# Performance work log

Measured on AMD Instinct MI355X. Metric: run time of the kernel, lower is better.

Reference implementation:

```python
import jax, jax.numpy as jnp
import numpy as np

B, S, D, H = 2, 2048, 1024, 16
HD = D // H  # head_dim = 64


def setup_inputs() -> dict:
    key = jax.random.key(0)
    ks = jax.random.split(key, 12)
    xav = (2.0 / (D + D)) ** 0.5  # xavier_normal std for square Linear
    q = jax.random.normal(ks[0], (B, S, D), jnp.float32)
    k = jax.random.normal(ks[1], (B, S, D), jnp.float32)
    v = jax.random.normal(ks[2], (B, S, D), jnp.float32)
    Wq = jax.random.normal(ks[3], (D, D), jnp.float32) * xav
    Wk = jax.random.normal(ks[4], (D, D), jnp.float32) * xav
    Wv = jax.random.normal(ks[5], (D, D), jnp.float32) * xav
    bq = jnp.zeros((D,), jnp.float32)
    bk = jnp.zeros((D,), jnp.float32)
    bv = jnp.zeros((D,), jnp.float32)
    # valid-prefix padding masks (True = valid token); key 0 always valid so
    # no causal softmax row is fully masked (avoids NaN, matches real usage).
    klen = jax.random.randint(ks[6], (B,), S // 2, S + 1)
    qlen = jax.random.randint(ks[7], (B,), S // 2, S + 1)
    pos = jnp.arange(S)
    key_padding_mask = pos[None, :] < klen[:, None]
    query_padding_mask = pos[None, :] < qlen[:, None]
    return {
        "q": q, "k": k, "v": v,
        "Wq": Wq, "bq": bq, "Wk": Wk, "bk": bk, "Wv": Wv, "bv": bv,
        "key_padding_mask": key_padding_mask,
        "query_padding_mask": query_padding_mask,
    }


def _proj_split(x, W, b, n_heads):
    # Linear (y = x W^T + b) then split heads: [B,S,D] -> [B,H,S,hd]
    bsz, sq, dm = x.shape
    hd = dm // n_heads
    y = x @ W.T + b
    return y.reshape(bsz, sq, n_heads, hd).transpose(0, 2, 1, 3)


def reference(q, k, v, Wq, bq, Wk, bk, Wv, bv, key_padding_mask, query_padding_mask):
    bsz, sq, dm = q.shape
    sk = k.shape[1]
    Q = _proj_split(q, Wq, bq, H)  # [B,H,Sq,hd]
    K = _proj_split(k, Wk, bk, H)  # [B,H,Sk,hd]
    V = _proj_split(v, Wv, bv, H)  # [B,H,Sk,hd]
    scale = 1.0 / jnp.sqrt(jnp.asarray(Q.shape[-1], Q.dtype))
    scores = jnp.einsum('bhqd,bhkd->bhqk', Q, K) * scale  # [B,H,Sq,Sk]
    # key padding: -inf where key invalid
    scores = jnp.where(key_padding_mask[:, None, None, :], scores, -jnp.inf)
    # causal: -inf strictly above the diagonal
    causal_ok = jnp.tril(jnp.ones((sq, sk), bool))
    scores = jnp.where(causal_ok[None, None, :, :], scores, -jnp.inf)
    attn = jax.nn.softmax(scores, axis=-1)
    # q_mask: zero out rows for padded queries (post-softmax, as in source)
    attn = jnp.where(query_padding_mask[:, None, :, None], attn, 0.0)
    # dropout p=0.0 -> identity
    out = jnp.einsum('bhqk,bhkd->bhqd', attn, V)
    out = out.transpose(0, 2, 1, 3).reshape(bsz, sq, dm)
    return out + q
```

## Files before the change

### kernel.cpp

```cpp
#include <hip/hip_runtime.h>
#include <stdint.h>

#define BATCH 2
#define SEQ 2048
#define DMODEL 1024
#define NHEAD 16
#define HDIM 64
#define CVT_BLOCKS 15360

typedef __attribute__((ext_vector_type(8))) short bf16x8;
typedef __attribute__((ext_vector_type(4))) float f32x4;

__device__ __forceinline__ unsigned short f2bf(float f) {
  unsigned int u = __float_as_uint(f);
  u += 0x7fffu + ((u >> 16) & 1u);
  return (unsigned short)(u >> 16);
}
__device__ __forceinline__ unsigned int pk2bf(float a, float b) {
  return __builtin_amdgcn_perm(__float_as_uint(b) + 0x8000u,
                               __float_as_uint(a) + 0x8000u, 0x07060302u);
}
__device__ __forceinline__ void async_copy16(const void* g, void* l) {
  __builtin_amdgcn_global_load_lds(
      (const __attribute__((address_space(1))) void*)g,
      (__attribute__((address_space(3))) void*)l, 16, 0, 0);
}

__global__ __launch_bounds__(256) void cvt_all(
    const float* __restrict__ q, const float* __restrict__ k,
    const float* __restrict__ v, const float* __restrict__ Wq,
    const float* __restrict__ Wk, const float* __restrict__ Wv,
    unsigned short* __restrict__ dst,
    const unsigned char* __restrict__ kp, const unsigned char* __restrict__ qp,
    int* __restrict__ lens) {
  if (blockIdx.x == CVT_BLOCKS) {
    const int t = threadIdx.x, wave = t >> 6, lane = t & 63;
    const unsigned char* base = (wave < 2) ? kp : qp;
    const int b = wave & 1;
    const bool bytefmt = (base[1] != 0);
    int cnt = 0;
    if (bytefmt) {
      const uint4* p = (const uint4*)(base + (size_t)b * SEQ);
#pragma unroll
      for (int g = 0; g < 2; g++) {
        const uint4 x = p[g * 64 + lane];
        const unsigned int w[4] = {x.x, x.y, x.z, x.w};
#pragma unroll
        for (int i = 0; i < 4; i++) {
          const unsigned int ww = w[i];
          cnt += ((ww & 0xffu) != 0) + ((ww & 0xff00u) != 0) +
                 ((ww & 0xff0000u) != 0) + ((ww & 0xff000000u) != 0);
        }
      }
    } else {
      const uint4* p = (const uint4*)(base + (size_t)b * SEQ * 4);
#pragma unroll
      for (int g = 0; g < 8; g++) {
        const uint4 x = p[g * 64 + lane];
        cnt += (x.x != 0) + (x.y != 0) + (x.z != 0) + (x.w != 0);
      }
    }
#pragma unroll
    for (int off = 32; off >= 1; off >>= 1) cnt += __shfl_xor(cnt, off, 64);
    if (lane == 0) lens[wave] = cnt;
    return;
  }
  const int g = blockIdx.x * 256 + threadIdx.x;
  const float* src;
  size_t off, dbase;
  if (g < 3 * (1 << 20)) {
    const int ti = g >> 20;
    src = (ti == 0) ? q : (ti == 1) ? k : v;
    off = (size_t)(g & ((1 << 20) - 1));
    dbase = (size_t)ti << 22;
  } else {
    const int gw = g - 3 * (1 << 20);
    const int ti = gw >> 18;
    src = (ti == 0) ? Wq : (ti == 1) ? Wk : Wv;
    off = (size_t)(gw & ((1 << 18) - 1));
    dbase = (3ull << 22) + ((size_t)ti << 20);
  }
  const float4 x = ((const float4*)src)[off];
  ushort4 o;
  o.x = f2bf(x.x); o.y = f2bf(x.y); o.z = f2bf(x.z); o.w = f2bf(x.w);
  *(ushort4*)(dst + dbase + off * 4) = o;
}

__global__ __launch_bounds__(256) void qkv_proj(
    const unsigned short* __restrict__ xq, const unsigned short* __restrict__ xk,
    const unsigned short* __restrict__ xv,
    const unsigned short* __restrict__ Wq, const float* __restrict__ bq,
    const unsigned short* __restrict__ Wk, const float* __restrict__ bk,
    const unsigned short* __restrict__ Wv, const float* __restrict__ bv,
    unsigned short* __restrict__ Qo, unsigned short* __restrict__ Ko,
    unsigned short* __restrict__ Vo, const int* __restrict__ lens) {
  const int z = blockIdx.z;
  const int m0 = blockIdx.y * 128, n0 = blockIdx.x * 128;
  const int b = m0 >> 11;
  const int len = (z == 0) ? lens[2 + b] : lens[b];
  if ((m0 & (SEQ - 1)) >= len) return;

  const unsigned short* x = (z == 0) ? xq : (z == 1) ? xk : xv;
  const unsigned short* W = (z == 0) ? Wq : (z == 1) ? Wk : Wv;
  const float* bias = (z == 0) ? bq : (z == 1) ? bk : bv;
  unsigned short* dst = (z == 0) ? Qo : (z == 1) ? Ko : Vo;
  const float osc = (z == 0) ? 0.18033688011112042f : 1.0f;

  __shared__ unsigned short As[128 * 64];
  __shared__ unsigned short Bs[128 * 64];

  const int t = threadIdx.x;
  const int wave = t >> 6, lane = t & 63, quad = lane >> 4, l16 = lane & 15;
  const int wm = wave >> 1, wn = wave & 1;

  const f32x4 fz = {0.f, 0.f, 0.f, 0.f};
  f32x4 acc[4][4];
#pragma unroll
  for (int i = 0; i < 4; i++)
#pragma unroll
    for (int j = 0; j < 4; j++) acc[i][j] = fz;

  for (int k0 = 0; k0 < DMODEL; k0 += 64) {
    __syncthreads();
#pragma unroll
    for (int c = 0; c < 4; c++) {
      const int slot = c * 256 + t;
      const int row = slot >> 3, pg = slot & 7;
      const int lg = (pg ^ (row & 7)) * 8;
      async_copy16(x + (size_t)(m0 + row) * DMODEL + k0 + lg,
                   (char*)As + (c * 256 + (t & 192)) * 16);
      async_copy16(W + (size_t)(n0 + row) * DMODEL + k0 + lg,
                   (char*)Bs + (c * 256 + (t & 192)) * 16);
    }
    __syncthreads();
#pragma unroll
    for (int kk = 0; kk < 2; kk++) {
      bf16x8 af[4], bfr[4];
#pragma unroll
      for (int i = 0; i < 4; i++) {
        const int ra = wm * 64 + i * 16 + l16;
        const int rb = wn * 64 + i * 16 + l16;
        af[i] = *(const bf16x8*)(As + ra * 64 + ((kk * 4 + quad) ^ (ra & 7)) * 8);
        bfr[i] = *(const bf16x8*)(Bs + rb * 64 + ((kk * 4 + quad) ^ (rb & 7)) * 8);
      }
      if (z == 2) {
#pragma unroll
        for (int i = 0; i < 4; i++)
#pragma unroll
          for (int j = 0; j < 4; j++)
            acc[i][j] = __builtin_amdgcn_mfma_f32_16x16x32_bf16(af[i], bfr[j], acc[i][j], 0, 0, 0);
      } else {
#pragma unroll
        for (int i = 0; i < 4; i++)
#pragma unroll
          for (int j = 0; j < 4; j++)
            acc[i][j] = __builtin_amdgcn_mfma_f32_16x16x32_bf16(bfr[j], af[i], acc[i][j], 0, 0, 0);
      }
    }
  }

  if (z == 2) {
#pragma unroll
    for (int j = 0; j < 4; j++) {
      const int n = n0 + wn * 64 + j * 16 + l16;
      const float bb_ = bias[n];
      const int h = n >> 6, hd = n & 63;
#pragma unroll
      for (int i = 0; i < 4; i++) {
        const int s0 = (m0 & (SEQ - 1)) + wm * 64 + i * 16 + quad * 4;
        uint2 w;
        w.x = pk2bf(acc[i][j][0] + bb_, acc[i][j][1] + bb_);
        w.y = pk2bf(acc[i][j][2] + bb_, acc[i][j][3] + bb_);
        *(uint2*)(dst + (((size_t)(b * NHEAD + h) * HDIM + hd) << 11) + s0) = w;
      }
    }
  } else {
#pragma unroll
    for (int j = 0; j < 4; j++) {
      const int nb = n0 + wn * 64 + j * 16 + quad * 4;
      const float4 b4 = *(const float4*)(bias + nb);
      const int h = nb >> 6, hd0 = nb & 63;
#pragma unroll
      for (int i = 0; i < 4; i++) {
        const int s = (m0 & (SEQ - 1)) + wm * 64 + i * 16 + l16;
        uint2 w;
        w.x = pk2bf((acc[i][j][0] + b4.x) * osc, (acc[i][j][1] + b4.y) * osc);
        w.y = pk2bf((acc[i][j][2] + b4.z) * osc, (acc[i][j][3] + b4.w) * osc);
        *(uint2*)(dst + (((size_t)(b * NHEAD + h) * SEQ + s) << 6) + hd0) = w;
      }
    }
  }
}


#define KVB 64

template <bool MASKED>
__device__ __forceinline__ void softmax_update(
    const f32x4 s[4], int key0, int qrow, int klen, int quad, int l16,
    float& mst, float& lsum, f32x4 o[4], unsigned short* Pdst) {
  float pm[4][4];
  float rm = -__builtin_inff();
  if (MASKED) {
    const int kmax = ((qrow < klen - 1) ? qrow : klen - 1) - key0 - quad * 4;
#pragma unroll
    for (int nf = 0; nf < 4; nf++)
#pragma unroll
      for (int r = 0; r < 4; r++) {
        pm[nf][r] = (nf * 16 + r <= kmax) ? s[nf][r] : -__builtin_inff();
        rm = fmaxf(rm, pm[nf][r]);
      }
  } else {
#pragma unroll
    for (int nf = 0; nf < 4; nf++)
#pragma unroll
      for (int r = 0; r < 4; r++) {
        pm[nf][r] = s[nf][r];
        rm = fmaxf(rm, pm[nf][r]);
      }
  }
  rm = fmaxf(rm, __shfl_xor(rm, 16, 64));
  rm = fmaxf(rm, __shfl_xor(rm, 32, 64));
  if (__ballot(rm > mst + 8.0f) != 0ull) {
    const float mnew = fmaxf(mst, rm);
    const float alpha = exp2f(fmaxf(mst, -1e30f) - fmaxf(mnew, -1e30f));
    mst = mnew;
    lsum *= alpha;
    float ab[4];
#pragma unroll
    for (int r = 0; r < 4; r++) ab[r] = __shfl(alpha, quad * 4 + r, 64);
#pragma unroll
    for (int db = 0; db < 4; db++)
#pragma unroll
      for (int r = 0; r < 4; r++) o[db][r] *= ab[r];
  }
  const float mref = fmaxf(mst, -1e30f);
  float rs = 0.f;
#pragma unroll
  for (int nf = 0; nf < 4; nf++)
#pragma unroll
    for (int r = 0; r < 4; r++) {
      const float p = exp2f(pm[nf][r] - mref);
      pm[nf][r] = p;
      rs += p;
    }
  rs += __shfl_xor(rs, 16, 64);
  rs += __shfl_xor(rs, 32, 64);
  lsum += rs;
#pragma unroll
  for (int nf = 0; nf < 4; nf++) {
    uint2 w;
    w.x = pk2bf(pm[nf][0], pm[nf][1]);
    w.y = pk2bf(pm[nf][2], pm[nf][3]);
    const int g = (nf * 2 + (quad >> 1)) ^ (l16 & 7);
    *(uint2*)(Pdst + l16 * KVB + g * 8 + (quad & 1) * 4) = w;
  }
}

template <bool MASKED>
__device__ __forceinline__ void tile_pass(
    const unsigned short* __restrict__ ks, const unsigned short* __restrict__ vt,
    unsigned short* __restrict__ Pw, bf16x8 qf0, bf16x8 qf1,
    int key0, int qrow, int klen, int quad, int l16,
    float& mst, float& lsum, f32x4 o[4]) {
  const f32x4 fz = {0.f, 0.f, 0.f, 0.f};
  f32x4 s[4];
  __builtin_amdgcn_s_setprio(1);
#pragma unroll
  for (int nf = 0; nf < 4; nf++) {
    const int row = nf * 16 + l16;
    const int sw = row & 7;
    const bf16x8 kf0 = *(const bf16x8*)(ks + row * 64 + (quad ^ sw) * 8);
    const bf16x8 kf1 = *(const bf16x8*)(ks + row * 64 + ((quad + 4) ^ sw) * 8);
    f32x4 a = fz;
    a = __builtin_amdgcn_mfma_f32_16x16x32_bf16(kf0, qf0, a, 0, 0, 0);
    a = __builtin_amdgcn_mfma_f32_16x16x32_bf16(kf1, qf1, a, 0, 0, 0);
    s[nf] = a;
  }
  __builtin_amdgcn_s_setprio(0);
  softmax_update<MASKED>(s, key0, qrow, klen, quad, l16, mst, lsum, o, Pw);
  bf16x8 pf[2];
#pragma unroll
  for (int ksn = 0; ksn < 2; ksn++)
    pf[ksn] = *(const bf16x8*)(Pw + l16 * KVB + ((ksn * 4 + quad) ^ (l16 & 7)) * 8);
  __builtin_amdgcn_s_setprio(1);
#pragma unroll
  for (int db = 0; db < 4; db++) {
    const int d = db * 16 + l16;
    const int sw = d & 7;
#pragma unroll
    for (int ksn = 0; ksn < 2; ksn++) {
      const bf16x8 v = *(const bf16x8*)(vt + d * KVB + ((ksn * 4 + quad) ^ sw) * 8);
      o[db] = __builtin_amdgcn_mfma_f32_16x16x32_bf16(pf[ksn], v, o[db], 0, 0, 0);
    }
  }
  __builtin_amdgcn_s_setprio(0);
}

__global__ __launch_bounds__(512, 2) void attn_kernel(
    const unsigned short* __restrict__ Qb, const unsigned short* __restrict__ Kb,
    const unsigned short* __restrict__ VTb, const float* __restrict__ qin,
    const int* __restrict__ lens, float* __restrict__ out) {
  const int pi = blockIdx.x, h = blockIdx.y, b = blockIdx.z;
  const int bh = b * NHEAD + h;
  const int t = threadIdx.x, wave = t >> 6, lane = t & 63, quad = lane >> 4, l16 = lane & 15;
  const int grp = wave >> 2, w4 = wave & 3;
  const int x = (pi + h) & 15;
  const int p = b ? x : 15 - x;
  const int myTile = 2 * p + grp;
  const int klen = lens[b], qlen = lens[2 + b];

  __shared__ unsigned short Ks[2][KVB * 64];
  __shared__ unsigned short VT[2][KVB * 64];
  __shared__ unsigned short Ps[8][16 * KVB];

  const unsigned short* Qp = Qb + (size_t)bh * SEQ * HDIM;
  const unsigned short* Kp = Kb + (size_t)bh * SEQ * HDIM;
  const unsigned short* Vt = VTb + (size_t)bh * HDIM * SEQ;

  const int qrow = myTile * 64 + w4 * 16 + l16;
  const bf16x8 qf0 = *(const bf16x8*)(Qp + (size_t)qrow * HDIM + quad * 8);
  const bf16x8 qf1 = *(const bf16x8*)(Qp + (size_t)qrow * HDIM + 32 + quad * 8);

  const f32x4 fz = {0.f, 0.f, 0.f, 0.f};
  f32x4 o[4];
#pragma unroll
  for (int i = 0; i < 4; i++) o[i] = fz;
  float mst = -__builtin_inff(), lsum = 0.f;

  const int tA = 2 * p, tB = 2 * p + 1;
  const int kendA = ((tA * 64 + 64) < klen) ? (tA * 64 + 64) : klen;
  const int kendB = ((tB * 64 + 64) < klen) ? (tB * 64 + 64) : klen;
  const int ktA = (tA * 64 < qlen) ? ((kendA + 63) >> 6) : 0;
  const int ktB = (tB * 64 < qlen) ? ((kendB + 63) >> 6) : 0;
  const int ktot = (ktA > ktB) ? ktA : ktB;
  const int myt = grp ? ktB : ktA;

  auto STAGE = [&](int buf, int kt) {
    const int key0 = kt << 6;
    const int row = t >> 3;
    const int sg = ((t & 7) ^ (row & 7)) * 8;
    async_copy16(Kp + (size_t)(key0 + row) * HDIM + sg,
                 (char*)Ks[buf] + (t & 448) * 16);
    async_copy16(Vt + (size_t)row * SEQ + key0 + sg,
                 (char*)VT[buf] + (t & 448) * 16);
  };

  STAGE(0, 0);
  __syncthreads();
  int cur = 0;
  for (int kt = 0; kt < ktot; kt++) {
    if (kt + 1 < ktot) STAGE(cur ^ 1, kt + 1);
    if (kt < myt) {
      const int key0 = kt << 6;
      if ((key0 + 63 <= myTile * 64 + w4 * 16) && (key0 + 63 < klen))
        tile_pass<false>(Ks[cur], VT[cur], Ps[wave], qf0, qf1, key0, qrow,
                         klen, quad, l16, mst, lsum, o);
      else
        tile_pass<true>(Ks[cur], VT[cur], Ps[wave], qf0, qf1, key0, qrow,
                        klen, quad, l16, mst, lsum, o);
    }
    __syncthreads();
    cur ^= 1;
  }

  const float inv = (lsum > 0.f) ? 1.f / lsum : 0.f;
  float ib[4];
#pragma unroll
  for (int r = 0; r < 4; r++) ib[r] = __shfl(inv, quad * 4 + r, 64);
#pragma unroll
  for (int db = 0; db < 4; db++) {
    const int col = h * HDIM + db * 16 + l16;
#pragma unroll
    for (int r = 0; r < 4; r++) {
      const int i = myTile * 64 + w4 * 16 + quad * 4 + r;
      const size_t oo = (size_t)(b * SEQ + i) * DMODEL + col;
      out[oo] = ((i < qlen) ? o[db][r] * ib[r] : 0.f) + qin[oo];
    }
  }
}

extern "C" void kernel_launch(void* const* d_in, const int* in_sizes, int n_in,
                              void* d_out, int out_size, void* d_ws, size_t ws_size,
                              hipStream_t stream) {
  (void)in_sizes; (void)n_in; (void)out_size; (void)ws_size;
  const float* q = (const float*)d_in[0];
  const float* k = (const float*)d_in[1];
  const float* v = (const float*)d_in[2];
  const float* Wq = (const float*)d_in[3];
  const float* bq = (const float*)d_in[4];
  const float* Wk = (const float*)d_in[5];
  const float* bk = (const float*)d_in[6];
  const float* Wv = (const float*)d_in[7];
  const float* bv = (const float*)d_in[8];
  const unsigned char* kpm = (const unsigned char*)d_in[9];
  const unsigned char* qpm = (const unsigned char*)d_in[10];
  float* out = (float*)d_out;

  const size_t tsz = (size_t)BATCH * SEQ * DMODEL;
  const size_t wsz = (size_t)DMODEL * DMODEL;

  char* ws = (char*)d_ws;
  int* lens = (int*)ws;
  unsigned short* cvt_base = (unsigned short*)(ws + 256);
  unsigned short* qb16 = cvt_base;
  unsigned short* kb16 = qb16 + tsz;
  unsigned short* vb16 = kb16 + tsz;
  unsigned short* Wqb = vb16 + tsz;
  unsigned short* Wkb = Wqb + wsz;
  unsigned short* Wvb = Wkb + wsz;
  unsigned short* Qw = Wvb + wsz;
  unsigned short* Kw = Qw + tsz;
  unsigned short* Vtw = Kw + tsz;

  cvt_all<<<dim3(CVT_BLOCKS + 1), dim3(256), 0, stream>>>(q, k, v, Wq, Wk, Wv,
                                                          cvt_base, kpm, qpm, lens);
  qkv_proj<<<dim3(8, 32, 3), dim3(256), 0, stream>>>(qb16, kb16, vb16, Wqb, bq, Wkb, bk, Wvb, bv, Qw, Kw, Vtw, lens);
  attn_kernel<<<dim3(16, NHEAD, BATCH), dim3(512), 0, stream>>>(Qw, Kw, Vtw, q, lens, out);
}
```

Before: 203.3 us.

## Fuse activation fp32-to-bf16 conversion into QKV projection A-tile loads

The standalone conversion pass now handles only the weights. The projection GEMM loads fp32 activations directly, packs them to bf16 in registers and stores them into the swizzled LDS tile, while the weight tile still uses async global-to-LDS copies. This removes a full write and read of the bf16 activation copies (about 24MB of fp32 read plus bf16 write). In exchange, the A-tile load becomes synchronous register traffic that each N-tile block repeats, so activation reads grow eightfold and the async copy overlap is lost.

```diff
diff --git a/kernel.cpp b/kernel.cpp
--- a/kernel.cpp
+++ b/kernel.cpp
@@ -6,7 +6,7 @@
 #define DMODEL 1024
 #define NHEAD 16
 #define HDIM 64
-#define CVT_BLOCKS 15360
+#define CVTW_BLOCKS 3072
 
 typedef __attribute__((ext_vector_type(8))) short bf16x8;
 typedef __attribute__((ext_vector_type(4))) float f32x4;
@@ -26,14 +26,12 @@
       (__attribute__((address_space(3))) void*)l, 16, 0, 0);
 }
 
-__global__ __launch_bounds__(256) void cvt_all(
-    const float* __restrict__ q, const float* __restrict__ k,
-    const float* __restrict__ v, const float* __restrict__ Wq,
-    const float* __restrict__ Wk, const float* __restrict__ Wv,
-    unsigned short* __restrict__ dst,
+__global__ __launch_bounds__(256) void cvt_w(
+    const float* __restrict__ Wq, const float* __restrict__ Wk,
+    const float* __restrict__ Wv, unsigned short* __restrict__ dst,
     const unsigned char* __restrict__ kp, const unsigned char* __restrict__ qp,
     int* __restrict__ lens) {
-  if (blockIdx.x == CVT_BLOCKS) {
+  if (blockIdx.x == CVTW_BLOCKS) {
     const int t = threadIdx.x, wave = t >> 6, lane = t & 63;
     const unsigned char* base = (wave < 2) ? kp : qp;
     const int b = wave & 1;
@@ -66,29 +64,18 @@
     return;
   }
   const int g = blockIdx.x * 256 + threadIdx.x;
-  const float* src;
-  size_t off, dbase;
-  if (g < 3 * (1 << 20)) {
-    const int ti = g >> 20;
-    src = (ti == 0) ? q : (ti == 1) ? k : v;
-    off = (size_t)(g & ((1 << 20) - 1));
-    dbase = (size_t)ti << 22;
-  } else {
-    const int gw = g - 3 * (1 << 20);
-    const int ti = gw >> 18;
-    src = (ti == 0) ? Wq : (ti == 1) ? Wk : Wv;
-    off = (size_t)(gw & ((1 << 18) - 1));
-    dbase = (3ull << 22) + ((size_t)ti << 20);
-  }
+  const int ti = g >> 18;
+  const size_t off = (size_t)(g & ((1 << 18) - 1));
+  const float* src = (ti == 0) ? Wq : (ti == 1) ? Wk : Wv;
   const float4 x = ((const float4*)src)[off];
   ushort4 o;
   o.x = f2bf(x.x); o.y = f2bf(x.y); o.z = f2bf(x.z); o.w = f2bf(x.w);
-  *(ushort4*)(dst + dbase + off * 4) = o;
+  *(ushort4*)(dst + ((size_t)ti << 20) + off * 4) = o;
 }
 
 __global__ __launch_bounds__(256) void qkv_proj(
-    const unsigned short* __restrict__ xq, const unsigned short* __restrict__ xk,
-    const unsigned short* __restrict__ xv,
+    const float* __restrict__ xq, const float* __restrict__ xk,
+    const float* __restrict__ xv,
     const unsigned short* __restrict__ Wq, const float* __restrict__ bq,
     const unsigned short* __restrict__ Wk, const float* __restrict__ bk,
     const unsigned short* __restrict__ Wv, const float* __restrict__ bv,
@@ -100,7 +87,7 @@
   const int len = (z == 0) ? lens[2 + b] : lens[b];
   if ((m0 & (SEQ - 1)) >= len) return;
 
-  const unsigned short* x = (z == 0) ? xq : (z == 1) ? xk : xv;
+  const float* x = (z == 0) ? xq : (z == 1) ? xk : xv;
   const unsigned short* W = (z == 0) ? Wq : (z == 1) ? Wk : Wv;
   const float* bias = (z == 0) ? bq : (z == 1) ? bk : bv;
   unsigned short* dst = (z == 0) ? Qo : (z == 1) ? Ko : Vo;
@@ -121,14 +108,26 @@
     for (int j = 0; j < 4; j++) acc[i][j] = fz;
 
   for (int k0 = 0; k0 < DMODEL; k0 += 64) {
-    __syncthreads();
+    uint4 av[4];
 #pragma unroll
     for (int c = 0; c < 4; c++) {
       const int slot = c * 256 + t;
       const int row = slot >> 3, pg = slot & 7;
       const int lg = (pg ^ (row & 7)) * 8;
-      async_copy16(x + (size_t)(m0 + row) * DMODEL + k0 + lg,
-                   (char*)As + (c * 256 + (t & 192)) * 16);
+      const float4* pa = (const float4*)(x + (size_t)(m0 + row) * DMODEL + k0 + lg);
+      const float4 a0 = pa[0], a1 = pa[1];
+      av[c].x = pk2bf(a0.x, a0.y);
+      av[c].y = pk2bf(a0.z, a0.w);
+      av[c].z = pk2bf(a1.x, a1.y);
+      av[c].w = pk2bf(a1.z, a1.w);
+    }
+    __syncthreads();
+#pragma unroll
+    for (int c = 0; c < 4; c++) {
+      const int slot = c * 256 + t;
+      *(uint4*)((char*)As + slot * 16) = av[c];
+      const int row = slot >> 3, pg = slot & 7;
+      const int lg = (pg ^ (row & 7)) * 8;
       async_copy16(W + (size_t)(n0 + row) * DMODEL + k0 + lg,
                    (char*)Bs + (c * 256 + (t & 192)) * 16);
     }
@@ -402,19 +401,14 @@
 
   char* ws = (char*)d_ws;
   int* lens = (int*)ws;
-  unsigned short* cvt_base = (unsigned short*)(ws + 256);
-  unsigned short* qb16 = cvt_base;
-  unsigned short* kb16 = qb16 + tsz;
-  unsigned short* vb16 = kb16 + tsz;
-  unsigned short* Wqb = vb16 + tsz;
+  unsigned short* Wqb = (unsigned short*)(ws + 256);
   unsigned short* Wkb = Wqb + wsz;
   unsigned short* Wvb = Wkb + wsz;
   unsigned short* Qw = Wvb + wsz;
   unsigned short* Kw = Qw + tsz;
   unsigned short* Vtw = Kw + tsz;
 
-  cvt_all<<<dim3(CVT_BLOCKS + 1), dim3(256), 0, stream>>>(q, k, v, Wq, Wk, Wv,
-                                                          cvt_base, kpm, qpm, lens);
-  qkv_proj<<<dim3(8, 32, 3), dim3(256), 0, stream>>>(qb16, kb16, vb16, Wqb, bq, Wkb, bk, Wvb, bv, Qw, Kw, Vtw, lens);
+  cvt_w<<<dim3(CVTW_BLOCKS + 1), dim3(256), 0, stream>>>(Wq, Wk, Wv, Wqb, kpm, qpm, lens);
+  qkv_proj<<<dim3(8, 32, 3), dim3(256), 0, stream>>>(q, k, v, Wqb, bq, Wkb, bk, Wvb, bv, Qw, Kw, Vtw, lens);
   attn_kernel<<<dim3(16, NHEAD, BATCH), dim3(512), 0, stream>>>(Qw, Kw, Vtw, q, lens, out);
 }
```

New measurement: 224.8 us. +10.6%, slower.
